# Performance work log

Hardware: AMD Instinct MI355X
Metric: run time of the kernel (lower is better)

The kernel has to match this reference:

```python
import jax, jax.numpy as jnp
import numpy as np

EMBED_DIM = 1024
N_HEADS = 16
HEAD_DIM = EMBED_DIM // N_HEADS


def setup_inputs() -> dict:
    key = jax.random.key(0)
    ks = jax.random.split(key, 5)
    B, T, C = 4, 2048, EMBED_DIM
    s = 0.02
    return {
        "x": jax.random.normal(ks[0], (B, T, C), dtype=jnp.float32),
        "w_qkv": jax.random.normal(ks[1], (C, 3 * C), dtype=jnp.float32) * s,
        "b_qkv": jnp.zeros((3 * C,), dtype=jnp.float32),
        "w_proj": jax.random.normal(ks[2], (C, C), dtype=jnp.float32) * s,
        "b_proj": jnp.zeros((C,), dtype=jnp.float32),
    }


def reference(x, w_qkv, b_qkv, w_proj, b_proj):
    B, T, C = x.shape
    H, D = N_HEADS, HEAD_DIM
    qkv = x @ w_qkv + b_qkv  # [B,T,3C]
    q, k, v = jnp.split(qkv, 3, axis=-1)
    # [B,H,T,D]
    q = q.reshape(B, T, H, D).transpose(0, 2, 1, 3)
    k = k.reshape(B, T, H, D).transpose(0, 2, 1, 3)
    v = v.reshape(B, T, H, D).transpose(0, 2, 1, 3)
    scale = jnp.asarray(D, x.dtype) ** -0.5
    att = jnp.einsum("bhqd,bhkd->bhqk", q, k) * scale  # [B,H,T,T]
    causal = jnp.tril(jnp.ones((T, T), dtype=bool))
    att = jnp.where(causal, att, jnp.asarray(-jnp.inf, att.dtype))
    att = jax.nn.softmax(att, axis=-1)
    out = jnp.einsum("bhqk,bhkd->bhqd", att, v)  # [B,H,T,D]
    out = out.transpose(0, 2, 1, 3).reshape(B, T, C)
    return out @ w_proj + b_proj
```

## Files before the change

### kernel.cpp

```cpp
#include <hip/hip_runtime.h>
#include <hip/hip_bf16.h>


typedef __bf16 bf16x8 __attribute__((ext_vector_type(8)));
typedef float f32x4 __attribute__((ext_vector_type(4)));
typedef unsigned short u16x8 __attribute__((ext_vector_type(8)));
typedef unsigned short u16x4 __attribute__((ext_vector_type(4)));
typedef unsigned int u32;

#define LOG2E 1.44269504088896340736f
#define NEG_INF (-__builtin_inff())

#define AS_GLOBAL(p) ((const __attribute__((address_space(1))) u32*)(p))
#define AS_LDS(p) ((__attribute__((address_space(3))) u32*)(p))

__device__ __forceinline__ unsigned short f2bf(float f) {
  unsigned int u = __builtin_bit_cast(unsigned int, f);
  u += 0x7fff + ((u >> 16) & 1);
  return (unsigned short)(u >> 16);
}

__device__ __forceinline__ u32 cvt_pk_bf16(float lo, float hi) {
  u32 r;
  asm("v_cvt_pk_bf16_f32 %0, %1, %2" : "=v"(r) : "v"(lo), "v"(hi));
  return r;
}

__device__ __forceinline__ bf16x8 ld_frag(const unsigned short* p) {
  return __builtin_bit_cast(bf16x8, *reinterpret_cast<const u16x8*>(p));
}

__global__ void k_convert(const float* __restrict__ in, unsigned short* __restrict__ out, int n4) {
  int i = blockIdx.x * blockDim.x + threadIdx.x;
  int stride = gridDim.x * blockDim.x;
  for (; i < n4; i += stride) {
    float4 v = reinterpret_cast<const float4*>(in)[i];
    u16x4 o = { f2bf(v.x), f2bf(v.y), f2bf(v.z), f2bf(v.w) };
    reinterpret_cast<u16x4*>(out)[i] = o;
  }
}

__global__ void k_transpose(const float* __restrict__ in, unsigned short* __restrict__ out,
                            int K, int N) {
  __shared__ float tile[32][33];
  int n0 = blockIdx.x * 32, k0 = blockIdx.y * 32;
  int tx = threadIdx.x & 31, ty = threadIdx.x >> 5;
#pragma unroll
  for (int i = 0; i < 4; i++)
    tile[ty + i * 8][tx] = in[(size_t)(k0 + ty + i * 8) * N + n0 + tx];
  __syncthreads();
#pragma unroll
  for (int i = 0; i < 4; i++)
    out[(size_t)(n0 + ty + i * 8) * K + k0 + tx] = f2bf(tile[tx][ty + i * 8]);
}

template <bool BF16_OUT>
__global__ __launch_bounds__(256) void k_gemm(
    const unsigned short* __restrict__ A, const unsigned short* __restrict__ Bt,
    const float* __restrict__ bias, void* __restrict__ Cv, int M, int N, int K) {
  constexpr int BK = 64;
  __shared__ unsigned short Asm[128][BK];
  __shared__ unsigned short Bsm[128][BK];
  const int tid = threadIdx.x;
  const int lane = tid & 63, w = tid >> 6;
  const int wr = w >> 1, wc = w & 1;
  const int brow = blockIdx.x * 128, bcol = blockIdx.y * 128;
  const int r0 = lane & 15, kq = lane >> 4;

  f32x4 acc[4][4] = {};

  const int srow = lane >> 3, scol = (lane & 7) * 8;

  for (int k0 = 0; k0 < K; k0 += BK) {
    __syncthreads();
#pragma unroll
    for (int q = 0; q < 4; q++) {
      int c = w * 4 + q;
      const unsigned short* ga = &A[(size_t)(brow + c * 8 + srow) * K + k0 + scol];
      const unsigned short* gb = &Bt[(size_t)(bcol + c * 8 + srow) * K + k0 + scol];
      __builtin_amdgcn_global_load_lds(AS_GLOBAL(ga), AS_LDS(&Asm[c * 8][0]), 16, 0, 0);
      __builtin_amdgcn_global_load_lds(AS_GLOBAL(gb), AS_LDS(&Bsm[c * 8][0]), 16, 0, 0);
    }
    __syncthreads();
#pragma unroll
    for (int c = 0; c < 2; c++) {
      bf16x8 af[4], bfr[4];
#pragma unroll
      for (int m = 0; m < 4; m++)
        af[m] = ld_frag(&Asm[wr * 64 + m * 16 + r0][c * 32 + kq * 8]);
#pragma unroll
      for (int n = 0; n < 4; n++)
        bfr[n] = ld_frag(&Bsm[wc * 64 + n * 16 + r0][c * 32 + kq * 8]);
      __builtin_amdgcn_s_setprio(1);
#pragma unroll
      for (int m = 0; m < 4; m++)
#pragma unroll
        for (int n = 0; n < 4; n++)
          acc[m][n] = __builtin_amdgcn_mfma_f32_16x16x32_bf16(af[m], bfr[n], acc[m][n], 0, 0, 0);
      __builtin_amdgcn_s_setprio(0);
    }
  }

  const int orow = kq * 4;
#pragma unroll
  for (int n = 0; n < 4; n++) {
#pragma unroll
    for (int m = 0; m < 4; m++) {
      int col = bcol + wc * 64 + n * 16 + r0;
      float bv = bias[col];
#pragma unroll
      for (int r = 0; r < 4; r++) {
        int row = brow + wr * 64 + m * 16 + orow + r;
        float v = acc[m][n][r] + bv;
        if (BF16_OUT)
          ((unsigned short*)Cv)[(size_t)row * N + col] = f2bf(v);
        else
          ((float*)Cv)[(size_t)row * N + col] = v;
      }
    }
  }
}

__global__ __launch_bounds__(256) void k_flash(const unsigned short* __restrict__ qkv,
                                               unsigned short* __restrict__ att, int T) {
  constexpr int C3 = 3072, C = 1024;
  __shared__ unsigned short Ksm[2][64][72];
  __shared__ unsigned short Vsm[2][64][72];

  const int tid = threadIdx.x, lane = tid & 63, w = tid >> 6;
  const int bh = blockIdx.x;
  const int qt = gridDim.y - 1 - blockIdx.y;
  const int b = bh >> 4, h = bh & 15;
  const int q0 = qt * 64;
  const int r0 = lane & 15, kq = lane >> 4;

  const size_t rowbase = (size_t)b * T * C3;

  bf16x8 qf[2];
  {
    const unsigned short* qp = &qkv[rowbase + (size_t)(q0 + w * 16 + r0) * C3 + h * 64];
    qf[0] = ld_frag(&qp[kq * 8]);
    qf[1] = ld_frag(&qp[32 + kq * 8]);
  }

  f32x4 accO[4] = {};
  float m_run = NEG_INF, l_run = 0.f;
  const int q_my = q0 + w * 16 + r0;

  const int stk = tid >> 3, sd8 = (tid & 7) * 8;

  u16x8 kreg[2], vreg[2];
  auto LOADT = [&](int kt) {
#pragma unroll
    for (int p = 0; p < 2; p++) {
      const size_t rb = rowbase + (size_t)(kt * 64 + p * 32 + stk) * C3 + h * 64 + sd8;
      kreg[p] = *reinterpret_cast<const u16x8*>(&qkv[rb + C]);
      vreg[p] = *reinterpret_cast<const u16x8*>(&qkv[rb + 2 * C]);
    }
  };
  auto WRITET = [&](int buf) {
#pragma unroll
    for (int p = 0; p < 2; p++) {
      int tkk = p * 32 + stk;
      *reinterpret_cast<u16x8*>(&Ksm[buf][tkk][sd8]) = kreg[p];
      int tkx = tkk ^ sd8;
#pragma unroll
      for (int i = 0; i < 8; i++) Vsm[buf][sd8 + i][tkx] = vreg[p][i];
    }
  };

  constexpr float SCL = 0.125f * LOG2E;
  auto TILE = [&](int buf, int k0, bool diag) {
    f32x4 st[4];
    __builtin_amdgcn_s_setprio(1);
#pragma unroll
    for (int s = 0; s < 4; s++) {
      f32x4 a = {};
      a = __builtin_amdgcn_mfma_f32_16x16x32_bf16(
          ld_frag(&Ksm[buf][s * 16 + r0][kq * 8]), qf[0], a, 0, 0, 0);
      a = __builtin_amdgcn_mfma_f32_16x16x32_bf16(
          ld_frag(&Ksm[buf][s * 16 + r0][32 + kq * 8]), qf[1], a, 0, 0, 0);
      st[s] = a;
    }
    __builtin_amdgcn_s_setprio(0);

    float sv[4][4];
    float mx = NEG_INF;
#pragma unroll
    for (int s = 0; s < 4; s++) {
#pragma unroll
      for (int r = 0; r < 4; r++) {
        float x = st[s][r] * SCL;
        if (diag) {
          int kg = k0 + s * 16 + kq * 4 + r;
          if (kg > q_my) x = NEG_INF;
        }
        sv[s][r] = x;
      }
      mx = fmaxf(fmaxf(mx, sv[s][0]), sv[s][1]);
      mx = fmaxf(fmaxf(mx, sv[s][2]), sv[s][3]);
    }
    mx = fmaxf(mx, __shfl_xor(mx, 16));
    mx = fmaxf(mx, __shfl_xor(mx, 32));

    if (__any(mx > m_run + 8.f)) {
      float mn = fmaxf(m_run, mx);
      float corr = exp2f(m_run - mn);
      m_run = mn;
      l_run *= corr;
      float cq[4];
#pragma unroll
      for (int r = 0; r < 4; r++) cq[r] = __shfl(corr, kq * 4 + r);
#pragma unroll
      for (int n = 0; n < 4; n++)
#pragma unroll
        for (int r = 0; r < 4; r++) accO[n][r] *= cq[r];
    }

    float pv[4][4];
    float ls = 0.f;
#pragma unroll
    for (int s = 0; s < 4; s++)
#pragma unroll
      for (int r = 0; r < 4; r++) {
        float p = exp2f(sv[s][r] - m_run);
        pv[s][r] = p;
        ls += p;
      }
    ls += __shfl_xor(ls, 16);
    ls += __shfl_xor(ls, 32);
    l_run += ls;

    __builtin_amdgcn_s_setprio(1);
#pragma unroll
    for (int t = 0; t < 2; t++) {
      u32 pd[4];
      pd[0] = cvt_pk_bf16(pv[2 * t][0], pv[2 * t][1]);
      pd[1] = cvt_pk_bf16(pv[2 * t][2], pv[2 * t][3]);
      pd[2] = cvt_pk_bf16(pv[2 * t + 1][0], pv[2 * t + 1][1]);
      pd[3] = cvt_pk_bf16(pv[2 * t + 1][2], pv[2 * t + 1][3]);
      bf16x8 pa = __builtin_bit_cast(bf16x8, *reinterpret_cast<u16x8*>(pd));
#pragma unroll
      for (int n = 0; n < 4; n++) {
        int d = n * 16 + r0;
        int swz = d & 56;
        const u16x4 lo = *reinterpret_cast<const u16x4*>(&Vsm[buf][d][(t * 32 + kq * 4) ^ swz]);
        const u16x4 hi = *reinterpret_cast<const u16x4*>(&Vsm[buf][d][(t * 32 + 16 + kq * 4) ^ swz]);
        u16x8 vb;
#pragma unroll
        for (int i = 0; i < 4; i++) { vb[i] = lo[i]; vb[4 + i] = hi[i]; }
        accO[n] = __builtin_amdgcn_mfma_f32_16x16x32_bf16(
            pa, __builtin_bit_cast(bf16x8, vb), accO[n], 0, 0, 0);
      }
    }
    __builtin_amdgcn_s_setprio(0);
  };

  int buf = 0;
  LOADT(0);
  WRITET(0);
  for (int kt = 0; kt < qt; kt++) {
    __syncthreads();
    LOADT(kt + 1);
    TILE(buf, kt * 64, false);
    WRITET(buf ^ 1);
    buf ^= 1;
  }
  __syncthreads();
  TILE(buf, qt * 64, true);

  float lq[4];
#pragma unroll
  for (int r = 0; r < 4; r++) lq[r] = __shfl(l_run, kq * 4 + r);
#pragma unroll
  for (int n = 0; n < 4; n++) {
#pragma unroll
    for (int r = 0; r < 4; r++) {
      int qrow = q0 + w * 16 + kq * 4 + r;
      float v = accO[n][r] / lq[r];
      att[((size_t)b * T + qrow) * C + h * 64 + n * 16 + r0] = f2bf(v);
    }
  }
}

extern "C" void kernel_launch(void* const* d_in, const int* in_sizes, int n_in,
                              void* d_out, int out_size, void* d_ws, size_t ws_size,
                              hipStream_t stream) {
  const float* x = (const float*)d_in[0];
  const float* w_qkv = (const float*)d_in[1];
  const float* b_qkv = (const float*)d_in[2];
  const float* w_proj = (const float*)d_in[3];
  const float* b_proj = (const float*)d_in[4];

  constexpr int B = 4, T = 2048, C = 1024, C3 = 3072;
  constexpr int M = B * T;

  unsigned short* x_bf = (unsigned short*)d_ws;
  unsigned short* wqkvT = x_bf + (size_t)M * C;
  unsigned short* wprojT = wqkvT + (size_t)C3 * C;
  unsigned short* qkv = wprojT + (size_t)C * C;
  unsigned short* att = qkv + (size_t)M * C3;

  hipLaunchKernelGGL(k_convert, dim3(2048), dim3(256), 0, stream, x, x_bf, M * C / 4);
  hipLaunchKernelGGL(k_transpose, dim3(C3 / 32, C / 32), dim3(256), 0, stream, w_qkv, wqkvT, C, C3);
  hipLaunchKernelGGL(k_transpose, dim3(C / 32, C / 32), dim3(256), 0, stream, w_proj, wprojT, C, C);
  hipLaunchKernelGGL((k_gemm<true>), dim3(M / 128, C3 / 128), dim3(256), 0, stream,
                     x_bf, wqkvT, b_qkv, (void*)qkv, M, C3, C);
  hipLaunchKernelGGL(k_flash, dim3(64, 32), dim3(256), 0, stream, qkv, att, T);
  hipLaunchKernelGGL((k_gemm<false>), dim3(M / 128, C / 128), dim3(256), 0, stream,
                     att, wprojT, b_proj, d_out, M, C, C);
}
```

Before: 191.4 us.

## Fold softmax scale into Q weights, swizzle GEMM blocks, defer row-sum reductions

Folds the attention scale times log2(e) into the Q columns of the transposed QKV weight and into a scaled copy of the bias. This removes the per-score multiply inside the flash kernel. The GEMM gets a block-index swizzle for better L2 reuse. The flash kernel now keeps the row sum as a per-lane vector and reduces it across lanes once at the end, shuffles for the max only when a rescale is needed, uses precomputed K/V pointer offsets, and multiplies by a reciprocal instead of dividing. Computing Q in bf16 after pre-scaling slightly changes rounding, and the lazy max check now uses per-lane maxima before the cross-lane reduction.

```diff
diff --git a/kernel.cpp b/kernel.cpp
--- a/kernel.cpp
+++ b/kernel.cpp
@@ -41,7 +41,7 @@
 }
 
 __global__ void k_transpose(const float* __restrict__ in, unsigned short* __restrict__ out,
-                            int K, int N) {
+                            int K, int N, int scaleN, float scl) {
   __shared__ float tile[32][33];
   int n0 = blockIdx.x * 32, k0 = blockIdx.y * 32;
   int tx = threadIdx.x & 31, ty = threadIdx.x >> 5;
@@ -50,8 +50,18 @@
     tile[ty + i * 8][tx] = in[(size_t)(k0 + ty + i * 8) * N + n0 + tx];
   __syncthreads();
 #pragma unroll
-  for (int i = 0; i < 4; i++)
-    out[(size_t)(n0 + ty + i * 8) * K + k0 + tx] = f2bf(tile[tx][ty + i * 8]);
+  for (int i = 0; i < 4; i++) {
+    int n = n0 + ty + i * 8;
+    float v = tile[tx][ty + i * 8];
+    if (n < scaleN) v *= scl;
+    out[(size_t)n * K + k0 + tx] = f2bf(v);
+  }
+}
+
+__global__ void k_scale_bias(const float* __restrict__ in, float* __restrict__ out,
+                             int n, int scaleN, float scl) {
+  int i = blockIdx.x * blockDim.x + threadIdx.x;
+  if (i < n) out[i] = (i < scaleN) ? in[i] * scl : in[i];
 }
 
 template <bool BF16_OUT>
@@ -64,7 +74,12 @@
   const int tid = threadIdx.x;
   const int lane = tid & 63, w = tid >> 6;
   const int wr = w >> 1, wc = w & 1;
-  const int brow = blockIdx.x * 128, bcol = blockIdx.y * 128;
+
+  int bid = blockIdx.y * gridDim.x + blockIdx.x;
+  int cpx = (gridDim.x * gridDim.y) >> 3;
+  int swz = (bid & 7) * cpx + (bid >> 3);
+  const int brow = (swz % gridDim.x) * 128, bcol = (swz / gridDim.x) * 128;
+
   const int r0 = lane & 15, kq = lane >> 4;
 
   f32x4 acc[4][4] = {};
@@ -144,18 +159,20 @@
   }
 
   f32x4 accO[4] = {};
-  float m_run = NEG_INF, l_run = 0.f;
+  f32x4 ls4 = {0.f, 0.f, 0.f, 0.f};
+  float m_run = NEG_INF;
   const int q_my = q0 + w * 16 + r0;
 
   const int stk = tid >> 3, sd8 = (tid & 7) * 8;
+  const unsigned short* kbase = &qkv[rowbase + (size_t)stk * C3 + h * 64 + sd8 + C];
+  constexpr size_t PSTRIDE = (size_t)32 * C3;
 
   u16x8 kreg[2], vreg[2];
-  auto LOADT = [&](int kt) {
+  auto LOADT = [&](size_t off) {
 #pragma unroll
     for (int p = 0; p < 2; p++) {
-      const size_t rb = rowbase + (size_t)(kt * 64 + p * 32 + stk) * C3 + h * 64 + sd8;
-      kreg[p] = *reinterpret_cast<const u16x8*>(&qkv[rb + C]);
-      vreg[p] = *reinterpret_cast<const u16x8*>(&qkv[rb + 2 * C]);
+      kreg[p] = *reinterpret_cast<const u16x8*>(kbase + off + p * PSTRIDE);
+      vreg[p] = *reinterpret_cast<const u16x8*>(kbase + off + p * PSTRIDE + C);
     }
   };
   auto WRITET = [&](int buf) {
@@ -169,45 +186,46 @@
     }
   };
 
-  constexpr float SCL = 0.125f * LOG2E;
   auto TILE = [&](int buf, int k0, bool diag) {
+    const unsigned short(*Ks)[72] = Ksm[buf];
+    const unsigned short(*Vs)[72] = Vsm[buf];
+
     f32x4 st[4];
     __builtin_amdgcn_s_setprio(1);
 #pragma unroll
     for (int s = 0; s < 4; s++) {
       f32x4 a = {};
-      a = __builtin_amdgcn_mfma_f32_16x16x32_bf16(
-          ld_frag(&Ksm[buf][s * 16 + r0][kq * 8]), qf[0], a, 0, 0, 0);
-      a = __builtin_amdgcn_mfma_f32_16x16x32_bf16(
-          ld_frag(&Ksm[buf][s * 16 + r0][32 + kq * 8]), qf[1], a, 0, 0, 0);
+      a = __builtin_amdgcn_mfma_f32_16x16x32_bf16(ld_frag(&Ks[s * 16 + r0][kq * 8]), qf[0], a, 0, 0, 0);
+      a = __builtin_amdgcn_mfma_f32_16x16x32_bf16(ld_frag(&Ks[s * 16 + r0][32 + kq * 8]), qf[1], a, 0, 0, 0);
       st[s] = a;
     }
     __builtin_amdgcn_s_setprio(0);
 
-    float sv[4][4];
-    float mx = NEG_INF;
-#pragma unroll
-    for (int s = 0; s < 4; s++) {
-#pragma unroll
-      for (int r = 0; r < 4; r++) {
-        float x = st[s][r] * SCL;
-        if (diag) {
+    f32x4 sv4[4];
+    if (diag) {
+#pragma unroll
+      for (int s = 0; s < 4; s++)
+#pragma unroll
+        for (int r = 0; r < 4; r++) {
           int kg = k0 + s * 16 + kq * 4 + r;
-          if (kg > q_my) x = NEG_INF;
+          sv4[s][r] = (kg > q_my) ? NEG_INF : st[s][r];
         }
-        sv[s][r] = x;
-      }
-      mx = fmaxf(fmaxf(mx, sv[s][0]), sv[s][1]);
-      mx = fmaxf(fmaxf(mx, sv[s][2]), sv[s][3]);
-    }
-    mx = fmaxf(mx, __shfl_xor(mx, 16));
-    mx = fmaxf(mx, __shfl_xor(mx, 32));
+    } else {
+#pragma unroll
+      for (int s = 0; s < 4; s++) sv4[s] = st[s];
+    }
+
+    f32x4 m4 = __builtin_elementwise_max(__builtin_elementwise_max(sv4[0], sv4[1]),
+                                         __builtin_elementwise_max(sv4[2], sv4[3]));
+    float mx = fmaxf(fmaxf(m4[0], m4[1]), fmaxf(m4[2], m4[3]));
 
     if (__any(mx > m_run + 8.f)) {
+      mx = fmaxf(mx, __shfl_xor(mx, 16));
+      mx = fmaxf(mx, __shfl_xor(mx, 32));
       float mn = fmaxf(m_run, mx);
       float corr = exp2f(m_run - mn);
       m_run = mn;
-      l_run *= corr;
+      ls4 *= corr;
       float cq[4];
 #pragma unroll
       for (int r = 0; r < 4; r++) cq[r] = __shfl(corr, kq * 4 + r);
@@ -217,35 +235,30 @@
         for (int r = 0; r < 4; r++) accO[n][r] *= cq[r];
     }
 
-    float pv[4][4];
-    float ls = 0.f;
-#pragma unroll
-    for (int s = 0; s < 4; s++)
-#pragma unroll
-      for (int r = 0; r < 4; r++) {
-        float p = exp2f(sv[s][r] - m_run);
-        pv[s][r] = p;
-        ls += p;
-      }
-    ls += __shfl_xor(ls, 16);
-    ls += __shfl_xor(ls, 32);
-    l_run += ls;
+    f32x4 pv4[4];
+#pragma unroll
+    for (int s = 0; s < 4; s++) {
+      f32x4 d = sv4[s] - m_run;
+      f32x4 p = { exp2f(d[0]), exp2f(d[1]), exp2f(d[2]), exp2f(d[3]) };
+      pv4[s] = p;
+      ls4 += p;
+    }
 
     __builtin_amdgcn_s_setprio(1);
 #pragma unroll
     for (int t = 0; t < 2; t++) {
       u32 pd[4];
-      pd[0] = cvt_pk_bf16(pv[2 * t][0], pv[2 * t][1]);
-      pd[1] = cvt_pk_bf16(pv[2 * t][2], pv[2 * t][3]);
-      pd[2] = cvt_pk_bf16(pv[2 * t + 1][0], pv[2 * t + 1][1]);
-      pd[3] = cvt_pk_bf16(pv[2 * t + 1][2], pv[2 * t + 1][3]);
+      pd[0] = cvt_pk_bf16(pv4[2 * t][0], pv4[2 * t][1]);
+      pd[1] = cvt_pk_bf16(pv4[2 * t][2], pv4[2 * t][3]);
+      pd[2] = cvt_pk_bf16(pv4[2 * t + 1][0], pv4[2 * t + 1][1]);
+      pd[3] = cvt_pk_bf16(pv4[2 * t + 1][2], pv4[2 * t + 1][3]);
       bf16x8 pa = __builtin_bit_cast(bf16x8, *reinterpret_cast<u16x8*>(pd));
 #pragma unroll
       for (int n = 0; n < 4; n++) {
         int d = n * 16 + r0;
-        int swz = d & 56;
-        const u16x4 lo = *reinterpret_cast<const u16x4*>(&Vsm[buf][d][(t * 32 + kq * 4) ^ swz]);
-        const u16x4 hi = *reinterpret_cast<const u16x4*>(&Vsm[buf][d][(t * 32 + 16 + kq * 4) ^ swz]);
+        int swzb = d & 56;
+        const u16x4 lo = *reinterpret_cast<const u16x4*>(&Vs[d][(t * 32 + kq * 4) ^ swzb]);
+        const u16x4 hi = *reinterpret_cast<const u16x4*>(&Vs[d][(t * 32 + 16 + kq * 4) ^ swzb]);
         u16x8 vb;
 #pragma unroll
         for (int i = 0; i < 4; i++) { vb[i] = lo[i]; vb[4 + i] = hi[i]; }
@@ -259,9 +272,11 @@
   int buf = 0;
   LOADT(0);
   WRITET(0);
+  size_t koff = (size_t)64 * C3;
   for (int kt = 0; kt < qt; kt++) {
     __syncthreads();
-    LOADT(kt + 1);
+    LOADT(koff);
+    koff += (size_t)64 * C3;
     TILE(buf, kt * 64, false);
     WRITET(buf ^ 1);
     buf ^= 1;
@@ -269,15 +284,18 @@
   __syncthreads();
   TILE(buf, qt * 64, true);
 
-  float lq[4];
-#pragma unroll
-  for (int r = 0; r < 4; r++) lq[r] = __shfl(l_run, kq * 4 + r);
+  float l_run = ls4[0] + ls4[1] + ls4[2] + ls4[3];
+  l_run += __shfl_xor(l_run, 16);
+  l_run += __shfl_xor(l_run, 32);
+  float lr[4];
+#pragma unroll
+  for (int r = 0; r < 4; r++) lr[r] = 1.f / __shfl(l_run, kq * 4 + r);
 #pragma unroll
   for (int n = 0; n < 4; n++) {
 #pragma unroll
     for (int r = 0; r < 4; r++) {
       int qrow = q0 + w * 16 + kq * 4 + r;
-      float v = accO[n][r] / lq[r];
+      float v = accO[n][r] * lr[r];
       att[((size_t)b * T + qrow) * C + h * 64 + n * 16 + r0] = f2bf(v);
     }
   }
@@ -294,18 +312,24 @@
 
   constexpr int B = 4, T = 2048, C = 1024, C3 = 3072;
   constexpr int M = B * T;
+  constexpr float SCL = 0.125f * LOG2E;
 
   unsigned short* x_bf = (unsigned short*)d_ws;
   unsigned short* wqkvT = x_bf + (size_t)M * C;
   unsigned short* wprojT = wqkvT + (size_t)C3 * C;
   unsigned short* qkv = wprojT + (size_t)C * C;
   unsigned short* att = qkv + (size_t)M * C3;
+  float* bias_s = (float*)(att + (size_t)M * C);
 
   hipLaunchKernelGGL(k_convert, dim3(2048), dim3(256), 0, stream, x, x_bf, M * C / 4);
-  hipLaunchKernelGGL(k_transpose, dim3(C3 / 32, C / 32), dim3(256), 0, stream, w_qkv, wqkvT, C, C3);
-  hipLaunchKernelGGL(k_transpose, dim3(C / 32, C / 32), dim3(256), 0, stream, w_proj, wprojT, C, C);
+  hipLaunchKernelGGL(k_transpose, dim3(C3 / 32, C / 32), dim3(256), 0, stream,
+                     w_qkv, wqkvT, C, C3, C, SCL);
+  hipLaunchKernelGGL(k_transpose, dim3(C / 32, C / 32), dim3(256), 0, stream,
+                     w_proj, wprojT, C, C, 0, 1.f);
+  hipLaunchKernelGGL(k_scale_bias, dim3((C3 + 255) / 256), dim3(256), 0, stream,
+                     b_qkv, bias_s, C3, C, SCL);
   hipLaunchKernelGGL((k_gemm<true>), dim3(M / 128, C3 / 128), dim3(256), 0, stream,
-                     x_bf, wqkvT, b_qkv, (void*)qkv, M, C3, C);
+                     x_bf, wqkvT, bias_s, (void*)qkv, M, C3, C);
   hipLaunchKernelGGL(k_flash, dim3(64, 32), dim3(256), 0, stream, qkv, att, T);
   hipLaunchKernelGGL((k_gemm<false>), dim3(M / 128, C / 128), dim3(256), 0, stream,
                      att, wprojT, b_proj, d_out, M, C, C);
```

Result: no change. 193.8 us (+1.2%).
